# Kernel optimization log

Hardware: AMD Instinct MI355X
Metric: run time of the kernel (lower is better)

Reference implementation:

```python
import jax, jax.numpy as jnp
import numpy as np

N, E, F, H, G, C = 50000, 600000, 128, 128, 500, 10
BN_EPS = 1e-5

def setup_inputs() -> dict:
    key = jax.random.key(0)
    ks = jax.random.split(key, 20)
    def lin(k, fan_in, shape):
        b = 1.0 / np.sqrt(fan_in)
        return jax.random.uniform(k, shape, jnp.float32, -b, b)
    inp = {
        'x': jax.random.normal(ks[0], (N, F), jnp.float32),
        'edge_index': jax.random.randint(ks[1], (2, E), 0, N, jnp.int64),
        'batch': jnp.sort(jax.random.randint(ks[2], (N,), 0, G, jnp.int64)),
        # conv1 MLP: Linear(F,H) -> BN(H) -> ReLU -> Dropout -> Linear(H,H) -> ReLU
        'W1a': lin(ks[3], F, (F, H)), 'b1a': lin(ks[4], F, (H,)),
        'g1': jnp.ones((H,), jnp.float32), 'be1': jnp.zeros((H,), jnp.float32),
        'm1': jnp.zeros((H,), jnp.float32), 'v1': jnp.ones((H,), jnp.float32),
        'W1b': lin(ks[5], H, (H, H)), 'b1b': lin(ks[6], H, (H,)),
        # conv2 MLP: Linear(H,H) -> ReLU -> BN(H) -> Dropout -> Linear(H,H) -> ReLU
        'W2a': lin(ks[7], H, (H, H)), 'b2a': lin(ks[8], H, (H,)),
        'g2': jnp.ones((H,), jnp.float32), 'be2': jnp.zeros((H,), jnp.float32),
        'm2': jnp.zeros((H,), jnp.float32), 'v2': jnp.ones((H,), jnp.float32),
        'W2b': lin(ks[9], H, (H, H)), 'b2b': lin(ks[10], H, (H,)),
        # heads
        'Wl1': lin(ks[11], 2 * H, (2 * H, H // 2)), 'bl1': lin(ks[12], 2 * H, (H // 2,)),
        'Wl2': lin(ks[13], H // 2, (H // 2, C)), 'bl2': lin(ks[14], H // 2, (C,)),
    }
    return inp

def _bn(h, g, b, m, v):
    return (h - m) * (g / jnp.sqrt(v + BN_EPS)) + b

def _gin_aggregate(x, src, dst):
    # out[i] = x[i] + sum_{j->i} x[j]  (GINConv with eps=0)
    return x + jax.ops.segment_sum(x[src], dst, num_segments=N)

def reference(x, edge_index, batch,
              W1a, b1a, g1, be1, m1, v1, W1b, b1b,
              W2a, b2a, g2, be2, m2, v2, W2b, b2b,
              Wl1, bl1, Wl2, bl2):
    src, dst = edge_index[0], edge_index[1]
    # conv1
    a1 = _gin_aggregate(x, src, dst)                       # [N, F]
    h1 = _bn(a1 @ W1a + b1a, g1, be1, m1, v1)
    h1 = jax.nn.relu(h1)                                   # dropout = identity (eval)
    h1 = jax.nn.relu(h1 @ W1b + b1b)                       # [N, H]
    # conv2
    a2 = _gin_aggregate(h1, src, dst)                      # [N, H]
    h2 = jax.nn.relu(a2 @ W2a + b2a)
    h2 = _bn(h2, g2, be2, m2, v2)
    h2 = jax.nn.relu(h2 @ W2b + b2b)                       # [N, H]
    # global add pool per graph
    p1 = jax.ops.segment_sum(h1, batch, num_segments=G)    # [G, H]
    p2 = jax.ops.segment_sum(h2, batch, num_segments=G)    # [G, H]
    z = jnp.concatenate((p1, p2), axis=1)                  # [G, 2H]
    z = jax.nn.relu(z @ Wl1 + bl1)
    return z @ Wl2 + bl2                                   # [G, C]
```

## Files before the change

### kernel.cpp

```cpp
#include <hip/hip_runtime.h>

#define N_NODES 50000
#define N_EDGES 600000
#define HDIM 128
#define NGRAPH 500
#define NCLASS 10
#define BN_EPS 1e-5f
#define KSLOT 64
#define KSTRIDE 72

typedef short short8 __attribute__((ext_vector_type(8)));
typedef float floatx4 __attribute__((ext_vector_type(4)));

__device__ __forceinline__ float bf2f(unsigned short u) {
    unsigned int v = ((unsigned int)u) << 16;
    return __uint_as_float(v);
}
__device__ __forceinline__ unsigned short f2bf(float f) {
    unsigned int u = __float_as_uint(f);
    unsigned int r = (u + 0x7fffu + ((u >> 16) & 1u)) >> 16;
    return (unsigned short)r;
}

#define NB_CAST 6250
#define NB_ZERO 196
#define NB_PREPW 256
#define NB_SETUP (NB_CAST + NB_ZERO + NB_PREPW + 1)

__global__ void k_setup(const float* __restrict__ x, unsigned short* __restrict__ xb,
                        int* __restrict__ cnt,
                        const float* __restrict__ W1a, const float* __restrict__ W1b,
                        const float* __restrict__ W2a, const float* __restrict__ W2b,
                        unsigned short* __restrict__ wpack,
                        const float* __restrict__ b1a, const float* __restrict__ g1,
                        const float* __restrict__ be1, const float* __restrict__ m1,
                        const float* __restrict__ v1, const float* __restrict__ b1b,
                        const float* __restrict__ b2a, const float* __restrict__ g2,
                        const float* __restrict__ be2, const float* __restrict__ m2,
                        const float* __restrict__ v2, const float* __restrict__ b2b,
                        float* __restrict__ ep) {
    int b = blockIdx.x;
    int t = threadIdx.x;
    if (b < NB_CAST) {
        int i = b * 256 + t;
        float4 v = ((const float4*)x)[i];
        ushort4 o;
        o.x = f2bf(v.x); o.y = f2bf(v.y); o.z = f2bf(v.z); o.w = f2bf(v.w);
        ((ushort4*)xb)[i] = o;
        return;
    }
    b -= NB_CAST;
    if (b < NB_ZERO) {
        int i = b * 256 + t;
        if (i < N_NODES) cnt[i] = 0;
        return;
    }
    b -= NB_ZERO;
    if (b < NB_PREPW) {
        int e = b * 256 + t;
        int w = e >> 14;
        int s_ = e & 16383;
        int j = s_ & 7;
        int m = (s_ >> 3) & 15;
        int q = (s_ >> 7) & 3;
        int ks = (s_ >> 9) & 3;
        int ct = (s_ >> 11) & 7;
        int n = ct * 16 + m;
        int k;
        float scale = 1.f;
        if (w == 0 || w == 2) {
            k = ks * 32 + q * 8 + j;
        } else {
            k = (ks * 2 + (j >> 2)) * 16 + q * 4 + (j & 3);
            if (w == 3) scale = g2[k] * rsqrtf(v2[k] + BN_EPS);
        }
        const float* W = (w == 0) ? W1a : (w == 1) ? W1b : (w == 2) ? W2a : W2b;
        wpack[e] = f2bf(W[k * 128 + n] * scale);
        return;
    }
    if (t < 128) {
        int j = t;
        float s1 = g1[j] * rsqrtf(v1[j] + BN_EPS);
        ep[0 * 256 + 0 + j]   = s1;
        ep[0 * 256 + 128 + j] = (b1a[j] - m1[j]) * s1 + be1[j];
        ep[1 * 256 + 0 + j]   = 1.f;
        ep[1 * 256 + 128 + j] = b2a[j];
        ep[512 + j] = b1b[j];
        float acc = b2b[j];
        for (int k = 0; k < 128; k++) {
            float s2k = g2[k] * rsqrtf(v2[k] + BN_EPS);
            acc += (be2[k] - m2[k] * s2k) * W2b[k * 128 + j];
        }
        ep[512 + 128 + j] = acc;
    }
}

__global__ void k_scatter(const int* __restrict__ src, const int* __restrict__ dst,
                          int* __restrict__ cnt, int* __restrict__ adj, int e) {
    int i = blockIdx.x * blockDim.x + threadIdx.x;
    if (i < e) {
        int d = dst[i];
        int p = atomicAdd(&cnt[d], 1);
        if (p < KSLOT) adj[d * KSTRIDE + p] = src[i];
    }
}

__global__ __launch_bounds__(256) void k_agg(const unsigned short* __restrict__ x,
                                             const int* __restrict__ cnt,
                                             const int* __restrict__ adj,
                                             unsigned short* __restrict__ out) {
    int g = blockIdx.x * 256 + threadIdx.x;
    int node = g >> 4;
    int m = g & 15;
    if (node >= N_NODES) return;

    int len = cnt[node];
    if (len > KSLOT) len = KSLOT;
    const int* ad = adj + node * KSTRIDE;

    int4 ra = *(const int4*)(ad);
    int4 rb = *(const int4*)(ad + 4);

    float self[8];
    {
        short8 sv = *(const short8*)(x + (size_t)node * 128 + m * 8);
        #pragma unroll
        for (int j = 0; j < 8; j++) self[j] = bf2f((unsigned short)sv[j]);
    }
    float acc[8];
    #pragma unroll
    for (int j = 0; j < 8; j++) acc[j] = self[j];

    int nb = (len + 7) >> 3;
    for (int b = 0; b < nb; b++) {
        int i = b * 8;
        int4 na = *(const int4*)(ad + i + 8);
        int4 nbv = *(const int4*)(ad + i + 12);
        int u0 = (i + 0 < len) ? ra.x : node;
        int u1 = (i + 1 < len) ? ra.y : node;
        int u2 = (i + 2 < len) ? ra.z : node;
        int u3 = (i + 3 < len) ? ra.w : node;
        int u4 = (i + 4 < len) ? rb.x : node;
        int u5 = (i + 5 < len) ? rb.y : node;
        int u6 = (i + 6 < len) ? rb.z : node;
        int u7 = (i + 7 < len) ? rb.w : node;
        short8 f0 = *(const short8*)(x + (size_t)u0 * 128 + m * 8);
        short8 f1 = *(const short8*)(x + (size_t)u1 * 128 + m * 8);
        short8 f2 = *(const short8*)(x + (size_t)u2 * 128 + m * 8);
        short8 f3 = *(const short8*)(x + (size_t)u3 * 128 + m * 8);
        short8 f4 = *(const short8*)(x + (size_t)u4 * 128 + m * 8);
        short8 f5 = *(const short8*)(x + (size_t)u5 * 128 + m * 8);
        short8 f6 = *(const short8*)(x + (size_t)u6 * 128 + m * 8);
        short8 f7 = *(const short8*)(x + (size_t)u7 * 128 + m * 8);
        #pragma unroll
        for (int j = 0; j < 8; j++) {
            float a = bf2f((unsigned short)f0[j]) + bf2f((unsigned short)f1[j]) +
                      bf2f((unsigned short)f2[j]) + bf2f((unsigned short)f3[j]);
            float c = bf2f((unsigned short)f4[j]) + bf2f((unsigned short)f5[j]) +
                      bf2f((unsigned short)f6[j]) + bf2f((unsigned short)f7[j]);
            acc[j] += a + c;
        }
        ra = na; rb = nbv;
    }
    float extra = (float)(nb * 8 - len);
    #pragma unroll
    for (int j = 0; j < 8; j++) acc[j] -= extra * self[j];

    short8 r;
    #pragma unroll
    for (int j = 0; j < 8; j++) r[j] = (short)f2bf(acc[j]);
    *(short8*)(out + (size_t)node * 128 + m * 8) = r;
}

__global__ __launch_bounds__(256, 4) void k_mlp(const unsigned short* __restrict__ A,
                                                const unsigned short* __restrict__ WaP,
                                                const unsigned short* __restrict__ WbP,
                                                const float* __restrict__ epi,
                                                const float* __restrict__ epf,
                                                unsigned short* __restrict__ Out, int n) {
    int t = threadIdx.x;
    int lane = t & 63;
    int w = t >> 6;
    int q = lane >> 4;
    int m = lane & 15;

    int base = blockIdx.x * 64 + w * 16;
    int node = base + m;
    if (node >= n) node = n - 1;

    short8 a1[4];
    #pragma unroll
    for (int s = 0; s < 4; s++)
        a1[s] = *(const short8*)(A + (size_t)node * 128 + s * 32 + q * 8);

    int lbase = lane * 8;

    floatx4 acc1[8];
    #pragma unroll
    for (int c = 0; c < 8; c++) acc1[c] = (floatx4)0.f;
    #pragma unroll
    for (int s = 0; s < 4; s++) {
        #pragma unroll
        for (int ct = 0; ct < 8; ct++) {
            short8 wf = *(const short8*)(WaP + (ct * 4 + s) * 512 + lbase);
            acc1[ct] = __builtin_amdgcn_mfma_f32_16x16x32_bf16(wf, a1[s], acc1[ct], 0, 0, 0);
        }
    }

    short8 a2[4];
    #pragma unroll
    for (int s = 0; s < 4; s++) {
        #pragma unroll
        for (int j = 0; j < 8; j++) {
            int ct = s * 2 + (j >> 2);
            int r = j & 3;
            int col = ct * 16 + q * 4 + r;
            float P = epi[col], Q = epi[128 + col];
            float v = fmaxf(fmaf(acc1[ct][r], P, Q), 0.f);
            a2[s][j] = (short)f2bf(v);
        }
    }

    floatx4 acc2[8];
    #pragma unroll
    for (int c = 0; c < 8; c++) acc2[c] = (floatx4)0.f;
    #pragma unroll
    for (int s = 0; s < 4; s++) {
        #pragma unroll
        for (int ct = 0; ct < 8; ct++) {
            short8 wf = *(const short8*)(WbP + (ct * 4 + s) * 512 + lbase);
            acc2[ct] = __builtin_amdgcn_mfma_f32_16x16x32_bf16(a2[s], wf, acc2[ct], 0, 0, 0);
        }
    }

    #pragma unroll
    for (int ct = 0; ct < 8; ct++) {
        int col = ct * 16 + m;
        float Qf = epf[col];
        #pragma unroll
        for (int r = 0; r < 4; r++) {
            int gr = base + q * 4 + r;
            if (gr < n)
                Out[(size_t)gr * 128 + col] = f2bf(fmaxf(acc2[ct][r] + Qf, 0.f));
        }
    }
}

__global__ void k_pool_head(const unsigned short* __restrict__ h1, const unsigned short* __restrict__ h2,
                            const int* __restrict__ batch, const float* __restrict__ Wl1,
                            const float* __restrict__ bl1, const float* __restrict__ Wl2,
                            const float* __restrict__ bl2, float* __restrict__ out) {
    int g = blockIdx.x;
    int t = threadIdx.x;
    int lo = 0, hi = N_NODES;
    while (lo < hi) { int mid = (lo + hi) >> 1; if (batch[mid] < g) lo = mid + 1; else hi = mid; }
    int start = lo;
    lo = 0; hi = N_NODES;
    while (lo < hi) { int mid = (lo + hi) >> 1; if (batch[mid] < g + 1) lo = mid + 1; else hi = mid; }
    int end = lo;

    int w = t >> 6, l = t & 63;
    const unsigned int* h = (w < 2) ? (const unsigned int*)h1 : (const unsigned int*)h2;
    int sub = w & 1;
    float ax = 0.f, ay = 0.f;
    int i = start + sub;
    for (; i + 6 < end; i += 8) {
        unsigned int v0 = h[(size_t)(i + 0) * 64 + l];
        unsigned int v1 = h[(size_t)(i + 2) * 64 + l];
        unsigned int v2 = h[(size_t)(i + 4) * 64 + l];
        unsigned int v3 = h[(size_t)(i + 6) * 64 + l];
        ax += bf2f((unsigned short)(v0 & 0xffff)) + bf2f((unsigned short)(v1 & 0xffff)) +
              bf2f((unsigned short)(v2 & 0xffff)) + bf2f((unsigned short)(v3 & 0xffff));
        ay += bf2f((unsigned short)(v0 >> 16)) + bf2f((unsigned short)(v1 >> 16)) +
              bf2f((unsigned short)(v2 >> 16)) + bf2f((unsigned short)(v3 >> 16));
    }
    for (; i < end; i += 2) {
        unsigned int v0 = h[(size_t)i * 64 + l];
        ax += bf2f((unsigned short)(v0 & 0xffff));
        ay += bf2f((unsigned short)(v0 >> 16));
    }

    __shared__ float red[4][128];
    __shared__ float zin[256];
    __shared__ float zmid[64];
    red[w][2 * l] = ax;
    red[w][2 * l + 1] = ay;
    __syncthreads();
    int mat = t >> 7, col = t & 127;
    zin[t] = red[mat * 2][col] + red[mat * 2 + 1][col];
    __syncthreads();
    if (t < 64) {
        float acc = bl1[t];
        #pragma unroll 8
        for (int k = 0; k < 256; k++) acc = fmaf(zin[k], Wl1[k * 64 + t], acc);
        zmid[t] = fmaxf(acc, 0.f);
    }
    __syncthreads();
    if (t < NCLASS) {
        float acc = bl2[t];
        #pragma unroll
        for (int j = 0; j < 64; j++) acc = fmaf(zmid[j], Wl2[j * 10 + t], acc);
        out[g * NCLASS + t] = acc;
    }
}


extern "C" void kernel_launch(void* const* d_in, const int* in_sizes, int n_in,
                              void* d_out, int out_size, void* d_ws, size_t ws_size,
                              hipStream_t stream) {
    const float* x   = (const float*)d_in[0];
    const int* eidx  = (const int*)d_in[1];
    const int* batch = (const int*)d_in[2];
    const float* W1a = (const float*)d_in[3];
    const float* b1a = (const float*)d_in[4];
    const float* g1  = (const float*)d_in[5];
    const float* be1 = (const float*)d_in[6];
    const float* m1  = (const float*)d_in[7];
    const float* v1  = (const float*)d_in[8];
    const float* W1b = (const float*)d_in[9];
    const float* b1b = (const float*)d_in[10];
    const float* W2a = (const float*)d_in[11];
    const float* b2a = (const float*)d_in[12];
    const float* g2  = (const float*)d_in[13];
    const float* be2 = (const float*)d_in[14];
    const float* m2  = (const float*)d_in[15];
    const float* v2  = (const float*)d_in[16];
    const float* W2b = (const float*)d_in[17];
    const float* b2b = (const float*)d_in[18];
    const float* Wl1 = (const float*)d_in[19];
    const float* bl1 = (const float*)d_in[20];
    const float* Wl2 = (const float*)d_in[21];
    const float* bl2 = (const float*)d_in[22];
    const int* srcv = eidx;
    const int* dstv = eidx + N_EDGES;

    char* ws = (char*)d_ws;
    size_t off = 0;
    auto alloc = [&](size_t bytes) -> void* {
        void* p = ws + off;
        off = (off + bytes + 255) & ~(size_t)255;
        return p;
    };
    int* cnt      = (int*)alloc(sizeof(int) * N_NODES);
    int* adj      = (int*)alloc(sizeof(int) * (size_t)N_NODES * KSTRIDE);
    float* ep     = (float*)alloc(sizeof(float) * 768);
    unsigned short* wpack = (unsigned short*)alloc(sizeof(unsigned short) * 4 * 16384);
    unsigned short* xb    = (unsigned short*)alloc(sizeof(unsigned short) * (size_t)N_NODES * HDIM);
    unsigned short* bufA  = (unsigned short*)alloc(sizeof(unsigned short) * (size_t)N_NODES * HDIM);
    unsigned short* bufB  = (unsigned short*)alloc(sizeof(unsigned short) * (size_t)N_NODES * HDIM);
    unsigned short* bufC  = (unsigned short*)alloc(sizeof(unsigned short) * (size_t)N_NODES * HDIM);
    (void)ws_size; (void)in_sizes; (void)n_in; (void)out_size;

    float* outp = (float*)d_out;

    k_setup<<<dim3(NB_SETUP), dim3(256), 0, stream>>>(
        x, xb, cnt, W1a, W1b, W2a, W2b, wpack,
        b1a, g1, be1, m1, v1, b1b, b2a, g2, be2, m2, v2, b2b, ep);
    k_scatter<<<dim3((N_EDGES + 255) / 256), dim3(256), 0, stream>>>(srcv, dstv, cnt, adj, N_EDGES);

    dim3 agrid((N_NODES * 16 + 255) / 256), ablk(256);
    dim3 mgrid((N_NODES + 63) / 64), mblk(256);

    k_agg<<<agrid, ablk, 0, stream>>>(xb, cnt, adj, bufA);
    k_mlp<<<mgrid, mblk, 0, stream>>>(bufA, wpack + 0 * 16384, wpack + 1 * 16384,
                                      ep + 0, ep + 512, bufC, N_NODES);
    k_agg<<<agrid, ablk, 0, stream>>>(bufC, cnt, adj, bufA);
    k_mlp<<<mgrid, mblk, 0, stream>>>(bufA, wpack + 2 * 16384, wpack + 3 * 16384,
                                      ep + 256, ep + 640, bufB, N_NODES);
    k_pool_head<<<dim3(NGRAPH), dim3(256), 0, stream>>>(bufC, bufB, batch, Wl1, bl1, Wl2, bl2, outp);
}
```

Measured before the change: 261.5 us.

## Fuse global add pooling into MLP epilogue and compress adjacency to 16-bit

Pooling moves into the k_mlp epilogue. Each block reduces its rows per graph through shared memory and atomically adds the result into a zeroed pool buffer, so the second MLP no longer writes its output and the pool kernel no longer re-reads both hidden tensors. The adjacency list is stored as 16-bit indices, halving its size and traffic in scatter and aggregation. The risks are extra __syncthreads per graph crossing in the MLP, float atomics that make the sums nondeterministic, and 16-bit indices that overflow for N=50000 only if N exceeds 65535.

```diff
diff --git a/kernel.cpp b/kernel.cpp
--- a/kernel.cpp
+++ b/kernel.cpp
@@ -10,6 +10,7 @@
 #define KSTRIDE 72
 
 typedef short short8 __attribute__((ext_vector_type(8)));
+typedef unsigned short ushort8v __attribute__((ext_vector_type(8)));
 typedef float floatx4 __attribute__((ext_vector_type(4)));
 
 __device__ __forceinline__ float bf2f(unsigned short u) {
@@ -25,10 +26,11 @@
 #define NB_CAST 6250
 #define NB_ZERO 196
 #define NB_PREPW 256
-#define NB_SETUP (NB_CAST + NB_ZERO + NB_PREPW + 1)
+#define NB_POOLZ 500
+#define NB_SETUP (NB_CAST + NB_ZERO + NB_PREPW + NB_POOLZ + 1)
 
 __global__ void k_setup(const float* __restrict__ x, unsigned short* __restrict__ xb,
-                        int* __restrict__ cnt,
+                        int* __restrict__ cnt, float* __restrict__ pool,
                         const float* __restrict__ W1a, const float* __restrict__ W1b,
                         const float* __restrict__ W2a, const float* __restrict__ W2b,
                         unsigned short* __restrict__ wpack,
@@ -78,6 +80,12 @@
         wpack[e] = f2bf(W[k * 128 + n] * scale);
         return;
     }
+    b -= NB_PREPW;
+    if (b < NB_POOLZ) {
+        int i = b * 256 + t;
+        pool[i] = 0.f;
+        return;
+    }
     if (t < 128) {
         int j = t;
         float s1 = g1[j] * rsqrtf(v1[j] + BN_EPS);
@@ -96,18 +104,18 @@
 }
 
 __global__ void k_scatter(const int* __restrict__ src, const int* __restrict__ dst,
-                          int* __restrict__ cnt, int* __restrict__ adj, int e) {
+                          int* __restrict__ cnt, unsigned short* __restrict__ adj, int e) {
     int i = blockIdx.x * blockDim.x + threadIdx.x;
     if (i < e) {
         int d = dst[i];
         int p = atomicAdd(&cnt[d], 1);
-        if (p < KSLOT) adj[d * KSTRIDE + p] = src[i];
+        if (p < KSLOT) adj[d * KSTRIDE + p] = (unsigned short)src[i];
     }
 }
 
 __global__ __launch_bounds__(256) void k_agg(const unsigned short* __restrict__ x,
                                              const int* __restrict__ cnt,
-                                             const int* __restrict__ adj,
+                                             const unsigned short* __restrict__ adj,
                                              unsigned short* __restrict__ out) {
     int g = blockIdx.x * 256 + threadIdx.x;
     int node = g >> 4;
@@ -116,10 +124,9 @@
 
     int len = cnt[node];
     if (len > KSLOT) len = KSLOT;
-    const int* ad = adj + node * KSTRIDE;
-
-    int4 ra = *(const int4*)(ad);
-    int4 rb = *(const int4*)(ad + 4);
+    const unsigned short* ad = adj + node * KSTRIDE;
+
+    ushort8v ra = *(const ushort8v*)(ad);
 
     float self[8];
     {
@@ -134,16 +141,15 @@
     int nb = (len + 7) >> 3;
     for (int b = 0; b < nb; b++) {
         int i = b * 8;
-        int4 na = *(const int4*)(ad + i + 8);
-        int4 nbv = *(const int4*)(ad + i + 12);
-        int u0 = (i + 0 < len) ? ra.x : node;
-        int u1 = (i + 1 < len) ? ra.y : node;
-        int u2 = (i + 2 < len) ? ra.z : node;
-        int u3 = (i + 3 < len) ? ra.w : node;
-        int u4 = (i + 4 < len) ? rb.x : node;
-        int u5 = (i + 5 < len) ? rb.y : node;
-        int u6 = (i + 6 < len) ? rb.z : node;
-        int u7 = (i + 7 < len) ? rb.w : node;
+        ushort8v na = *(const ushort8v*)(ad + i + 8);
+        int u0 = (i + 0 < len) ? (int)ra[0] : node;
+        int u1 = (i + 1 < len) ? (int)ra[1] : node;
+        int u2 = (i + 2 < len) ? (int)ra[2] : node;
+        int u3 = (i + 3 < len) ? (int)ra[3] : node;
+        int u4 = (i + 4 < len) ? (int)ra[4] : node;
+        int u5 = (i + 5 < len) ? (int)ra[5] : node;
+        int u6 = (i + 6 < len) ? (int)ra[6] : node;
+        int u7 = (i + 7 < len) ? (int)ra[7] : node;
         short8 f0 = *(const short8*)(x + (size_t)u0 * 128 + m * 8);
         short8 f1 = *(const short8*)(x + (size_t)u1 * 128 + m * 8);
         short8 f2 = *(const short8*)(x + (size_t)u2 * 128 + m * 8);
@@ -160,7 +166,7 @@
                       bf2f((unsigned short)f6[j]) + bf2f((unsigned short)f7[j]);
             acc[j] += a + c;
         }
-        ra = na; rb = nbv;
+        ra = na;
     }
     float extra = (float)(nb * 8 - len);
     #pragma unroll
@@ -177,14 +183,18 @@
                                                 const unsigned short* __restrict__ WbP,
                                                 const float* __restrict__ epi,
                                                 const float* __restrict__ epf,
+                                                const int* __restrict__ batch,
+                                                float* __restrict__ poolc,
                                                 unsigned short* __restrict__ Out, int n) {
+    __shared__ float ps[16][132];
     int t = threadIdx.x;
     int lane = t & 63;
     int w = t >> 6;
     int q = lane >> 4;
     int m = lane & 15;
 
-    int base = blockIdx.x * 64 + w * 16;
+    int rowbase0 = blockIdx.x * 64;
+    int base = rowbase0 + w * 16;
     int node = base + m;
     if (node >= n) node = n - 1;
 
@@ -235,72 +245,75 @@
 
     #pragma unroll
     for (int ct = 0; ct < 8; ct++) {
-        int col = ct * 16 + m;
-        float Qf = epf[col];
+        float Qf = epf[ct * 16 + m];
+        #pragma unroll
+        for (int r = 0; r < 4; r++) acc2[ct][r] = fmaxf(acc2[ct][r] + Qf, 0.f);
+    }
+
+    if (Out) {
+        #pragma unroll
+        for (int ct = 0; ct < 8; ct++) {
+            int col = ct * 16 + m;
+            #pragma unroll
+            for (int r = 0; r < 4; r++) {
+                int gr = base + q * 4 + r;
+                if (gr < n)
+                    Out[(size_t)gr * 128 + col] = f2bf(acc2[ct][r]);
+            }
+        }
+    }
+
+    int mygid[4];
+    #pragma unroll
+    for (int r = 0; r < 4; r++) {
+        int gr = base + q * 4 + r;
+        mygid[r] = (gr < n) ? batch[gr] : -1;
+    }
+    int lastrow = rowbase0 + 63;
+    if (lastrow > n - 1) lastrow = n - 1;
+    int g0 = batch[rowbase0];
+    int g1 = batch[lastrow];
+    for (int g = g0; g <= g1; g++) {
+        float pv[8];
+        #pragma unroll
+        for (int ct = 0; ct < 8; ct++) pv[ct] = 0.f;
         #pragma unroll
         for (int r = 0; r < 4; r++) {
-            int gr = base + q * 4 + r;
-            if (gr < n)
-                Out[(size_t)gr * 128 + col] = f2bf(fmaxf(acc2[ct][r] + Qf, 0.f));
-        }
-    }
-}
-
-__global__ void k_pool_head(const unsigned short* __restrict__ h1, const unsigned short* __restrict__ h2,
-                            const int* __restrict__ batch, const float* __restrict__ Wl1,
-                            const float* __restrict__ bl1, const float* __restrict__ Wl2,
-                            const float* __restrict__ bl2, float* __restrict__ out) {
+            if (mygid[r] == g) {
+                #pragma unroll
+                for (int ct = 0; ct < 8; ct++) pv[ct] += acc2[ct][r];
+            }
+        }
+        #pragma unroll
+        for (int ct = 0; ct < 8; ct++) ps[w * 4 + q][ct * 16 + m] = pv[ct];
+        __syncthreads();
+        if (t < 128) {
+            float s = 0.f;
+            #pragma unroll
+            for (int k = 0; k < 16; k++) s += ps[k][t];
+            atomicAdd(&poolc[g * 256 + t], s);
+        }
+        __syncthreads();
+    }
+}
+
+__global__ void k_head(const float* __restrict__ pool, const float* __restrict__ Wl1,
+                       const float* __restrict__ bl1, const float* __restrict__ Wl2,
+                       const float* __restrict__ bl2, float* __restrict__ out) {
     int g = blockIdx.x;
     int t = threadIdx.x;
-    int lo = 0, hi = N_NODES;
-    while (lo < hi) { int mid = (lo + hi) >> 1; if (batch[mid] < g) lo = mid + 1; else hi = mid; }
-    int start = lo;
-    lo = 0; hi = N_NODES;
-    while (lo < hi) { int mid = (lo + hi) >> 1; if (batch[mid] < g + 1) lo = mid + 1; else hi = mid; }
-    int end = lo;
-
-    int w = t >> 6, l = t & 63;
-    const unsigned int* h = (w < 2) ? (const unsigned int*)h1 : (const unsigned int*)h2;
-    int sub = w & 1;
-    float ax = 0.f, ay = 0.f;
-    int i = start + sub;
-    for (; i + 6 < end; i += 8) {
-        unsigned int v0 = h[(size_t)(i + 0) * 64 + l];
-        unsigned int v1 = h[(size_t)(i + 2) * 64 + l];
-        unsigned int v2 = h[(size_t)(i + 4) * 64 + l];
-        unsigned int v3 = h[(size_t)(i + 6) * 64 + l];
-        ax += bf2f((unsigned short)(v0 & 0xffff)) + bf2f((unsigned short)(v1 & 0xffff)) +
-              bf2f((unsigned short)(v2 & 0xffff)) + bf2f((unsigned short)(v3 & 0xffff));
-        ay += bf2f((unsigned short)(v0 >> 16)) + bf2f((unsigned short)(v1 >> 16)) +
-              bf2f((unsigned short)(v2 >> 16)) + bf2f((unsigned short)(v3 >> 16));
-    }
-    for (; i < end; i += 2) {
-        unsigned int v0 = h[(size_t)i * 64 + l];
-        ax += bf2f((unsigned short)(v0 & 0xffff));
-        ay += bf2f((unsigned short)(v0 >> 16));
-    }
-
-    __shared__ float red[4][128];
-    __shared__ float zin[256];
     __shared__ float zmid[64];
-    red[w][2 * l] = ax;
-    red[w][2 * l + 1] = ay;
-    __syncthreads();
-    int mat = t >> 7, col = t & 127;
-    zin[t] = red[mat * 2][col] + red[mat * 2 + 1][col];
-    __syncthreads();
-    if (t < 64) {
-        float acc = bl1[t];
-        #pragma unroll 8
-        for (int k = 0; k < 256; k++) acc = fmaf(zin[k], Wl1[k * 64 + t], acc);
-        zmid[t] = fmaxf(acc, 0.f);
-    }
+    const float* z = pool + g * 256;
+    float acc = bl1[t];
+    #pragma unroll 8
+    for (int k = 0; k < 256; k++) acc = fmaf(z[k], Wl1[k * 64 + t], acc);
+    zmid[t] = fmaxf(acc, 0.f);
     __syncthreads();
     if (t < NCLASS) {
-        float acc = bl2[t];
-        #pragma unroll
-        for (int j = 0; j < 64; j++) acc = fmaf(zmid[j], Wl2[j * 10 + t], acc);
-        out[g * NCLASS + t] = acc;
+        float a = bl2[t];
+        #pragma unroll
+        for (int j = 0; j < 64; j++) a = fmaf(zmid[j], Wl2[j * 10 + t], a);
+        out[g * NCLASS + t] = a;
     }
 }
 
@@ -342,19 +355,19 @@
         return p;
     };
     int* cnt      = (int*)alloc(sizeof(int) * N_NODES);
-    int* adj      = (int*)alloc(sizeof(int) * (size_t)N_NODES * KSTRIDE);
+    unsigned short* adj = (unsigned short*)alloc(sizeof(unsigned short) * (size_t)N_NODES * KSTRIDE);
     float* ep     = (float*)alloc(sizeof(float) * 768);
+    float* pool   = (float*)alloc(sizeof(float) * NGRAPH * 256);
     unsigned short* wpack = (unsigned short*)alloc(sizeof(unsigned short) * 4 * 16384);
     unsigned short* xb    = (unsigned short*)alloc(sizeof(unsigned short) * (size_t)N_NODES * HDIM);
     unsigned short* bufA  = (unsigned short*)alloc(sizeof(unsigned short) * (size_t)N_NODES * HDIM);
-    unsigned short* bufB  = (unsigned short*)alloc(sizeof(unsigned short) * (size_t)N_NODES * HDIM);
     unsigned short* bufC  = (unsigned short*)alloc(sizeof(unsigned short) * (size_t)N_NODES * HDIM);
     (void)ws_size; (void)in_sizes; (void)n_in; (void)out_size;
 
     float* outp = (float*)d_out;
 
     k_setup<<<dim3(NB_SETUP), dim3(256), 0, stream>>>(
-        x, xb, cnt, W1a, W1b, W2a, W2b, wpack,
+        x, xb, cnt, pool, W1a, W1b, W2a, W2b, wpack,
         b1a, g1, be1, m1, v1, b1b, b2a, g2, be2, m2, v2, b2b, ep);
     k_scatter<<<dim3((N_EDGES + 255) / 256), dim3(256), 0, stream>>>(srcv, dstv, cnt, adj, N_EDGES);
 
@@ -363,9 +376,9 @@
 
     k_agg<<<agrid, ablk, 0, stream>>>(xb, cnt, adj, bufA);
     k_mlp<<<mgrid, mblk, 0, stream>>>(bufA, wpack + 0 * 16384, wpack + 1 * 16384,
-                                      ep + 0, ep + 512, bufC, N_NODES);
+                                      ep + 0, ep + 512, batch, pool + 0, bufC, N_NODES);
     k_agg<<<agrid, ablk, 0, stream>>>(bufC, cnt, adj, bufA);
     k_mlp<<<mgrid, mblk, 0, stream>>>(bufA, wpack + 2 * 16384, wpack + 3 * 16384,
-                                      ep + 256, ep + 640, bufB, N_NODES);
-    k_pool_head<<<dim3(NGRAPH), dim3(256), 0, stream>>>(bufC, bufB, batch, Wl1, bl1, Wl2, bl2, outp);
-}
+                                      ep + 256, ep + 640, batch, pool + 128, nullptr, N_NODES);
+    k_head<<<dim3(NGRAPH), dim3(64), 0, stream>>>(pool, Wl1, bl1, Wl2, bl2, outp);
+}
```

New measurement: 241.4 us. -7.7%, faster.
